# Optimization experiments

Hardware: AMD Instinct MI355X
Metric: run time of the kernel (lower is better)

Reference implementation:

```python
import jax, jax.numpy as jnp
import numpy as np

B, F, T, D, U = 4096, 256, 128, 6, 16  # batch, features, n_trees, depth, units
NB = 2 ** D  # number of leaf bins


def sparsemax(z):
    # sparsemax over the last axis (matches tfa.activations.sparsemax default axis=-1)
    d = z.shape[-1]
    z_sorted = -jnp.sort(-z, axis=-1)
    k = jnp.arange(1, d + 1, dtype=z.dtype)
    z_cumsum = jnp.cumsum(z_sorted, axis=-1)
    support = (1 + k * z_sorted) > z_cumsum
    k_z = jnp.sum(support, axis=-1, keepdims=True)
    tau = (jnp.take_along_axis(z_cumsum, k_z - 1, axis=-1) - 1.0) / k_z.astype(z.dtype)
    return jnp.maximum(z - tau, 0.0)


def bin_codes_1hot(depth):
    # (depth, 2^depth, 2) one-hot binary codes, as in build()
    idx = np.arange(2 ** depth)
    off = 2 ** np.arange(depth)
    codes = (idx[None, :] // off[:, None]) % 2  # (depth, 2^depth)
    return jnp.asarray(np.stack([codes, 1 - codes], axis=-1), dtype=jnp.float32)


def setup_inputs() -> dict:
    key = jax.random.key(0)
    k1, k2, k3, k4 = jax.random.split(key, 4)
    x = jax.random.normal(k1, (B, F), dtype=jnp.float32)
    feature_selection_logits = jax.random.normal(k2, (F, T, D), dtype=jnp.float32)
    feature_thresholds = 0.1 * jax.random.normal(k3, (T, D), dtype=jnp.float32)
    log_temperatures = jnp.zeros((T, D), dtype=jnp.float32)
    response = jax.random.normal(k4, (T, U, NB), dtype=jnp.float32)
    return {
        "x": x,
        "feature_selection_logits": feature_selection_logits,
        "feature_thresholds": feature_thresholds,
        "log_temperatures": log_temperatures,
        "response": response,
    }


def reference(x, feature_selection_logits, feature_thresholds, log_temperatures, response):
    depth = feature_thresholds.shape[-1]
    codes = bin_codes_1hot(depth)  # (D, 2^D, 2)
    # feature selection
    selectors = sparsemax(feature_selection_logits)          # (F, T, D)
    feature_values = jnp.einsum('bi,ind->bnd', x, selectors)  # (B, T, D)
    # sigmoid-style binarization via sparsemoid
    tl = (feature_values - feature_thresholds) * jnp.exp(-log_temperatures)
    tl = jnp.stack([-tl, tl], axis=-1)                        # (B, T, D, 2)
    bins = jnp.clip(0.5 * tl + 0.5, 0.0, 1.0)                 # sparsemoid
    # one-hot bin matching and product over depth
    bin_matches = jnp.einsum('btds,dcs->btdc', bins, codes)   # (B, T, D, 2^D)
    response_weights = jnp.prod(bin_matches, axis=-2)         # (B, T, 2^D)
    out = jnp.einsum('bnd,ncd->bnc', response_weights, response)  # (B, T, U)
    return jnp.sum(out, axis=1)                               # (B, U)
```

## Files before the change

### kernel.cpp

```cpp
#include <hip/hip_runtime.h>
#include <math.h>

#define B_  4096
#define F_  256
#define T_  128
#define D_  6
#define U_  16
#define NB_ 64
#define N_  (T_ * D_)

typedef __attribute__((ext_vector_type(8))) short bf16x8;
typedef __attribute__((ext_vector_type(4))) float f32x4;

__device__ __forceinline__ short f2b(float f) {
    union { float f; unsigned u; } v; v.f = f;
    unsigned r = (v.u + 0x7FFFu + ((v.u >> 16) & 1u)) >> 16;
    return (short)r;
}
__device__ __forceinline__ float clamp01(float x) {
    return fminf(fmaxf(x, 0.f), 1.f);
}

__global__ __launch_bounds__(256) void prep(const float* __restrict__ fsl,
                                            const float* __restrict__ th,
                                            const float* __restrict__ lt,
                                            const float* __restrict__ resp,
                                            unsigned short* __restrict__ sel_t,
                                            unsigned short* __restrict__ resp_b,
                                            float2* __restrict__ tsc) {
    int bid = blockIdx.x, tid = threadIdx.x;
    if (bid < 128) {
        int r = bid * 256 + tid;
        const float* zp = fsl + (size_t)r * 6;
        float v0 = zp[0], v1 = zp[1], v2 = zp[2], v3 = zp[3], v4 = zp[4], v5 = zp[5];
        float s0 = v0, s1 = v1, s2 = v2, s3 = v3, s4 = v4, s5 = v5;
#define CE(a, b) { float hi_ = fmaxf(a, b), lo_ = fminf(a, b); a = hi_; b = lo_; }
        CE(s0, s1) CE(s2, s3) CE(s4, s5)
        CE(s1, s2) CE(s3, s4)
        CE(s0, s1) CE(s2, s3) CE(s4, s5)
        CE(s1, s2) CE(s3, s4)
        CE(s0, s1) CE(s2, s3) CE(s4, s5)
        CE(s1, s2) CE(s3, s4)
#undef CE
        float cum = 0.f, num = 0.f, kz = 1.f;
        cum += s0; num = cum; kz = 1.f;
        cum += s1; if (1.f + 2.f * s1 > cum) { num = cum; kz = 2.f; }
        cum += s2; if (1.f + 3.f * s2 > cum) { num = cum; kz = 3.f; }
        cum += s3; if (1.f + 4.f * s3 > cum) { num = cum; kz = 4.f; }
        cum += s4; if (1.f + 5.f * s4 > cum) { num = cum; kz = 5.f; }
        cum += s5; if (1.f + 6.f * s5 > cum) { num = cum; kz = 6.f; }
        float tau = (num - 1.f) / kz;
        int f = r >> 7, t = r & 127;
        unsigned short* o = sel_t + f;
        o[(t * 6 + 0) * 256] = (unsigned short)f2b(fmaxf(v0 - tau, 0.f));
        o[(t * 6 + 1) * 256] = (unsigned short)f2b(fmaxf(v1 - tau, 0.f));
        o[(t * 6 + 2) * 256] = (unsigned short)f2b(fmaxf(v2 - tau, 0.f));
        o[(t * 6 + 3) * 256] = (unsigned short)f2b(fmaxf(v3 - tau, 0.f));
        o[(t * 6 + 4) * 256] = (unsigned short)f2b(fmaxf(v4 - tau, 0.f));
        o[(t * 6 + 5) * 256] = (unsigned short)f2b(fmaxf(v5 - tau, 0.f));
    } else if (bid < 256) {
        int i = (bid - 128) * 256 + tid;
        float4 v = *(const float4*)(resp + (size_t)4 * i);
        ushort4 o;
        o.x = (unsigned short)f2b(v.x); o.y = (unsigned short)f2b(v.y);
        o.z = (unsigned short)f2b(v.z); o.w = (unsigned short)f2b(v.w);
        *(ushort4*)(resp_b + (size_t)4 * i) = o;
    } else {
        for (int i = tid; i < N_; i += 256) {
            float s = expf(-lt[i]);
            tsc[i] = make_float2(s, -th[i] * s);
        }
    }
}

__global__ __launch_bounds__(256) void gemm_fv(const float* __restrict__ x,
                                               const unsigned short* __restrict__ sel_t,
                                               float* __restrict__ fv) {
    int tid = threadIdx.x;
    int lane = tid & 63;
    int wave = tid >> 6;
    int tile = blockIdx.x * 4 + wave;
    int mT = tile & 127;
    int nT = tile >> 7;
    int m0 = mT * 32, n0 = nT * 32;
    int lm = lane & 15;
    int kq = lane >> 4;
    f32x4 acc[2][2] = {};
#pragma unroll
    for (int ks = 0; ks < 8; ks++) {
        int k0 = ks * 32 + kq * 8;
        bf16x8 a[2], b[2];
#pragma unroll
        for (int mt = 0; mt < 2; mt++) {
            const float* ap = x + (size_t)(m0 + mt * 16 + lm) * F_ + k0;
            float4 f0 = *(const float4*)ap;
            float4 f1 = *(const float4*)(ap + 4);
            bf16x8 t;
            t[0] = f2b(f0.x); t[1] = f2b(f0.y); t[2] = f2b(f0.z); t[3] = f2b(f0.w);
            t[4] = f2b(f1.x); t[5] = f2b(f1.y); t[6] = f2b(f1.z); t[7] = f2b(f1.w);
            a[mt] = t;
        }
#pragma unroll
        for (int nt = 0; nt < 2; nt++) {
            const unsigned short* bp = sel_t + (size_t)(n0 + nt * 16 + lm) * F_ + k0;
            b[nt] = *(const bf16x8*)bp;
        }
#pragma unroll
        for (int mt = 0; mt < 2; mt++)
#pragma unroll
            for (int nt = 0; nt < 2; nt++)
                acc[mt][nt] = __builtin_amdgcn_mfma_f32_16x16x32_bf16(a[mt], b[nt], acc[mt][nt], 0, 0, 0);
    }
    int rb = kq * 4;
#pragma unroll
    for (int mt = 0; mt < 2; mt++)
#pragma unroll
        for (int nt = 0; nt < 2; nt++)
#pragma unroll
            for (int r = 0; r < 4; r++)
                fv[(size_t)(m0 + mt * 16 + rb + r) * N_ + n0 + nt * 16 + lm] = acc[mt][nt][r];
}

__global__ __launch_bounds__(512) void leafsum_mfma(const float* __restrict__ fv,
                                                    const unsigned short* __restrict__ resp_b,
                                                    const float2* __restrict__ tsc,
                                                    float* __restrict__ out) {
    __shared__ float red[8][16][17];
    int tid = threadIdx.x;
    int lane = tid & 63;
    int wave = tid >> 6;
    int b0 = blockIdx.x * 16;
    int lm = lane & 15;
    int kq = lane >> 4;
    int q0 = kq & 1, q1 = kq >> 1;
    const float* fvb = fv + (size_t)(b0 + lm) * N_;
    f32x4 acc = {};
    for (int t = wave; t < T_; t += 8) {
        float bp[6], bn[6];
#pragma unroll
        for (int d = 0; d < 6; d++) {
            float2 so = tsc[t * 6 + d];
            float tl = fmaf(fvb[t * 6 + d], so.x, so.y);
            bp[d] = clamp01(fmaf(tl, 0.5f, 0.5f));
            bn[d] = clamp01(fmaf(tl, -0.5f, 0.5f));
        }
        float p01[4] = { bp[0] * bp[1], bn[0] * bp[1], bp[0] * bn[1], bn[0] * bn[1] };
        float p3[8];
#pragma unroll
        for (int j = 0; j < 8; j++) p3[j] = p01[j & 3] * ((j & 4) ? bn[2] : bp[2]);
        float t34 = (q0 ? bn[3] : bp[3]) * (q1 ? bn[4] : bp[4]);
        float w0 = t34 * bp[5], w1 = t34 * bn[5];
        bf16x8 a0, a1;
#pragma unroll
        for (int j = 0; j < 8; j++) {
            a0[j] = f2b(p3[j] * w0);
            a1[j] = f2b(p3[j] * w1);
        }
        const unsigned short* rbp = resp_b + (size_t)t * (U_ * NB_) + lm * NB_ + kq * 8;
        bf16x8 br0 = *(const bf16x8*)rbp;
        bf16x8 br1 = *(const bf16x8*)(rbp + 32);
        acc = __builtin_amdgcn_mfma_f32_16x16x32_bf16(a0, br0, acc, 0, 0, 0);
        acc = __builtin_amdgcn_mfma_f32_16x16x32_bf16(a1, br1, acc, 0, 0, 0);
    }
#pragma unroll
    for (int r = 0; r < 4; r++) red[wave][kq * 4 + r][lm] = acc[r];
    __syncthreads();
    if (tid < 256) {
        int row = tid >> 4, col = tid & 15;
        float s = 0.f;
#pragma unroll
        for (int w = 0; w < 8; w++) s += red[w][row][col];
        out[(size_t)(b0 + row) * U_ + col] = s;
    }
}

extern "C" void kernel_launch(void* const* d_in, const int* in_sizes, int n_in,
                              void* d_out, int out_size, void* d_ws, size_t ws_size,
                              hipStream_t stream) {
    const float* x    = (const float*)d_in[0];
    const float* fsl  = (const float*)d_in[1];
    const float* th   = (const float*)d_in[2];
    const float* lt   = (const float*)d_in[3];
    const float* resp = (const float*)d_in[4];
    float* out = (float*)d_out;

    char* w = (char*)d_ws;
    float*          fv     = (float*)w;
    unsigned short* sel_t  = (unsigned short*)(w + 12582912);
    unsigned short* resp_b = (unsigned short*)(w + 12976128);
    float2*         tsc    = (float2*)(w + 13238272);

    prep<<<dim3(257), dim3(256), 0, stream>>>(fsl, th, lt, resp, sel_t, resp_b, tsc);
    gemm_fv<<<dim3(768), dim3(256), 0, stream>>>(x, sel_t, fv);
    leafsum_mfma<<<dim3(B_ / 16), dim3(512), 0, stream>>>(fv, resp_b, tsc, out);
}
```

Before: 104.0 us.

## Fuse feature-value GEMM into leaf-sum kernel via shared-memory tile

Merges the x·selectors GEMM into the leaf-sum kernel. Each 512-thread block computes its 16-row feature-value tile (16×768) with MFMA into LDS, then runs the leaf-weight MFMA stage from LDS. This removes the 12 MB fv round trip through global memory and one kernel launch. In exchange each block reads the full 384 KB bf16 selector matrix (L2-resident), and the ~49 KB LDS footprint may limit occupancy.

```diff
diff --git a/kernel.cpp b/kernel.cpp
--- a/kernel.cpp
+++ b/kernel.cpp
@@ -73,58 +73,15 @@
     }
 }
 
-__global__ __launch_bounds__(256) void gemm_fv(const float* __restrict__ x,
-                                               const unsigned short* __restrict__ sel_t,
-                                               float* __restrict__ fv) {
-    int tid = threadIdx.x;
-    int lane = tid & 63;
-    int wave = tid >> 6;
-    int tile = blockIdx.x * 4 + wave;
-    int mT = tile & 127;
-    int nT = tile >> 7;
-    int m0 = mT * 32, n0 = nT * 32;
-    int lm = lane & 15;
-    int kq = lane >> 4;
-    f32x4 acc[2][2] = {};
-#pragma unroll
-    for (int ks = 0; ks < 8; ks++) {
-        int k0 = ks * 32 + kq * 8;
-        bf16x8 a[2], b[2];
-#pragma unroll
-        for (int mt = 0; mt < 2; mt++) {
-            const float* ap = x + (size_t)(m0 + mt * 16 + lm) * F_ + k0;
-            float4 f0 = *(const float4*)ap;
-            float4 f1 = *(const float4*)(ap + 4);
-            bf16x8 t;
-            t[0] = f2b(f0.x); t[1] = f2b(f0.y); t[2] = f2b(f0.z); t[3] = f2b(f0.w);
-            t[4] = f2b(f1.x); t[5] = f2b(f1.y); t[6] = f2b(f1.z); t[7] = f2b(f1.w);
-            a[mt] = t;
-        }
-#pragma unroll
-        for (int nt = 0; nt < 2; nt++) {
-            const unsigned short* bp = sel_t + (size_t)(n0 + nt * 16 + lm) * F_ + k0;
-            b[nt] = *(const bf16x8*)bp;
-        }
-#pragma unroll
-        for (int mt = 0; mt < 2; mt++)
-#pragma unroll
-            for (int nt = 0; nt < 2; nt++)
-                acc[mt][nt] = __builtin_amdgcn_mfma_f32_16x16x32_bf16(a[mt], b[nt], acc[mt][nt], 0, 0, 0);
-    }
-    int rb = kq * 4;
-#pragma unroll
-    for (int mt = 0; mt < 2; mt++)
-#pragma unroll
-        for (int nt = 0; nt < 2; nt++)
-#pragma unroll
-            for (int r = 0; r < 4; r++)
-                fv[(size_t)(m0 + mt * 16 + rb + r) * N_ + n0 + nt * 16 + lm] = acc[mt][nt][r];
-}
+#define FVP 772
 
-__global__ __launch_bounds__(512) void leafsum_mfma(const float* __restrict__ fv,
-                                                    const unsigned short* __restrict__ resp_b,
-                                                    const float2* __restrict__ tsc,
-                                                    float* __restrict__ out) {
+__global__ __launch_bounds__(512) void fused_gemm_leafsum(
+        const float* __restrict__ x,
+        const unsigned short* __restrict__ sel_t,
+        const unsigned short* __restrict__ resp_b,
+        const float2* __restrict__ tsc,
+        float* __restrict__ out) {
+    __shared__ float fvs[16][FVP];
     __shared__ float red[8][16][17];
     int tid = threadIdx.x;
     int lane = tid & 63;
@@ -132,15 +89,43 @@
     int b0 = blockIdx.x * 16;
     int lm = lane & 15;
     int kq = lane >> 4;
+
+    {
+        f32x4 acc[6] = {};
+#pragma unroll
+        for (int ks = 0; ks < 8; ks++) {
+            int k0 = ks * 32 + kq * 8;
+            const float* ap = x + (size_t)(b0 + lm) * F_ + k0;
+            float4 f0 = *(const float4*)ap;
+            float4 f1 = *(const float4*)(ap + 4);
+            bf16x8 a;
+            a[0] = f2b(f0.x); a[1] = f2b(f0.y); a[2] = f2b(f0.z); a[3] = f2b(f0.w);
+            a[4] = f2b(f1.x); a[5] = f2b(f1.y); a[6] = f2b(f1.z); a[7] = f2b(f1.w);
+#pragma unroll
+            for (int i = 0; i < 6; i++) {
+                int n = (wave * 6 + i) * 16 + lm;
+                bf16x8 b = *(const bf16x8*)(sel_t + (size_t)n * F_ + k0);
+                acc[i] = __builtin_amdgcn_mfma_f32_16x16x32_bf16(a, b, acc[i], 0, 0, 0);
+            }
+        }
+#pragma unroll
+        for (int i = 0; i < 6; i++) {
+            int n0 = (wave * 6 + i) * 16;
+#pragma unroll
+            for (int r = 0; r < 4; r++)
+                fvs[kq * 4 + r][n0 + lm] = acc[i][r];
+        }
+    }
+    __syncthreads();
+
+    f32x4 acc = {};
     int q0 = kq & 1, q1 = kq >> 1;
-    const float* fvb = fv + (size_t)(b0 + lm) * N_;
-    f32x4 acc = {};
     for (int t = wave; t < T_; t += 8) {
         float bp[6], bn[6];
 #pragma unroll
         for (int d = 0; d < 6; d++) {
             float2 so = tsc[t * 6 + d];
-            float tl = fmaf(fvb[t * 6 + d], so.x, so.y);
+            float tl = fmaf(fvs[lm][t * 6 + d], so.x, so.y);
             bp[d] = clamp01(fmaf(tl, 0.5f, 0.5f));
             bn[d] = clamp01(fmaf(tl, -0.5f, 0.5f));
         }
@@ -185,12 +170,10 @@
     float* out = (float*)d_out;
 
     char* w = (char*)d_ws;
-    float*          fv     = (float*)w;
-    unsigned short* sel_t  = (unsigned short*)(w + 12582912);
-    unsigned short* resp_b = (unsigned short*)(w + 12976128);
-    float2*         tsc    = (float2*)(w + 13238272);
+    unsigned short* sel_t  = (unsigned short*)w;
+    unsigned short* resp_b = (unsigned short*)(w + 393216);
+    float2*         tsc    = (float2*)(w + 655360);
 
     prep<<<dim3(257), dim3(256), 0, stream>>>(fsl, th, lt, resp, sel_t, resp_b, tsc);
-    gemm_fv<<<dim3(768), dim3(256), 0, stream>>>(x, sel_t, fv);
-    leafsum_mfma<<<dim3(B_ / 16), dim3(512), 0, stream>>>(fv, resp_b, tsc, out);
+    fused_gemm_leafsum<<<dim3(B_ / 16), dim3(512), 0, stream>>>(x, sel_t, resp_b, tsc, out);
 }
```

New measurement: 89.40 us. 1.16x faster.
